# Kernel optimization log

Hardware: AMD Instinct MI355X
Metric: run time of the kernel (lower is better)

Reference implementation:

```python
import jax, jax.numpy as jnp
import numpy as np

EMBED = 256
HEADS = 8
LEVELS = 4
POINTS = 4
HD = EMBED // HEADS  # 32


def _bilinear_sample(v, grid):
    """torch.F.grid_sample(mode='bilinear', padding_mode='zeros', align_corners=False).
    v: (B, C, H, W); grid: (B, Q, P, 2) with xy coords in [-1, 1].
    Returns (B, C, Q, P).
    """
    B, C, H, W = v.shape
    x = (grid[..., 0] + 1.0) * (W * 0.5) - 0.5
    y = (grid[..., 1] + 1.0) * (H * 0.5) - 0.5
    x0f = jnp.floor(x)
    y0f = jnp.floor(y)
    wx = x - x0f
    wy = y - y0f
    x0 = x0f.astype(jnp.int32)
    y0 = y0f.astype(jnp.int32)
    vf = v.reshape(B, C, H * W)

    def corner(xi, yi, w):
        valid = (xi >= 0) & (xi < W) & (yi >= 0) & (yi < H)
        idx = jnp.clip(yi, 0, H - 1) * W + jnp.clip(xi, 0, W - 1)  # (B, Q, P)
        g = jax.vmap(lambda vb, ib: jnp.take(vb, ib, axis=1))(vf, idx.reshape(B, -1))
        g = g.reshape(B, C, idx.shape[1], idx.shape[2])  # (B, C, Q, P)
        return g * (w * valid.astype(v.dtype))[:, None]

    return (corner(x0, y0, (1 - wx) * (1 - wy))
            + corner(x0 + 1, y0, wx * (1 - wy))
            + corner(x0, y0 + 1, (1 - wx) * wy)
            + corner(x0 + 1, y0 + 1, wx * wy))


def setup_inputs() -> dict:
    key = jax.random.key(0)
    ks = jax.random.split(key, 16)
    N, Q, D = 2, 8192, EMBED
    inp = {
        'query': jax.random.normal(ks[0], (N, Q, D), jnp.float32),
        'feat0': jax.random.normal(ks[1], (N, D, 64, 64), jnp.float32),
        'feat1': jax.random.normal(ks[2], (N, D, 32, 32), jnp.float32),
        'feat2': jax.random.normal(ks[3], (N, D, 16, 16), jnp.float32),
        'feat3': jax.random.normal(ks[4], (N, D, 8, 8), jnp.float32),
        'reference_points': jax.random.uniform(ks[5], (N, Q, 2), jnp.float32),
        # params stored as (in, out); equivalent math to torch Linear's x @ W.T + b
        'W_off': jax.random.normal(ks[6], (D, HEADS * LEVELS * POINTS * 2), jnp.float32) * 0.01,
        'b_off': jax.random.normal(ks[7], (HEADS * LEVELS * POINTS * 2,), jnp.float32) * 0.01,
        'W_attn': jax.random.normal(ks[8], (D, HEADS * LEVELS * POINTS), jnp.float32) * 0.02,
        'b_attn': jax.random.normal(ks[9], (HEADS * LEVELS * POINTS,), jnp.float32) * 0.02,
        'W_val': jax.random.normal(ks[10], (D, D), jnp.float32) * (1.0 / np.sqrt(D)),
        'b_val': jnp.zeros((D,), jnp.float32),
        'W_out': jax.random.normal(ks[11], (D, D), jnp.float32) * (1.0 / np.sqrt(D)),
        'b_out': jnp.zeros((D,), jnp.float32),
    }
    return inp


def reference(query, feat0, feat1, feat2, feat3, reference_points,
              W_off, b_off, W_attn, b_attn, W_val, b_val, W_out, b_out):
    feats = [feat0, feat1, feat2, feat3]
    N, Q, D = query.shape
    # offset / attention-weight projections
    off = (query @ W_off + b_off).reshape(N, Q, HEADS, LEVELS, POINTS, 2)
    attn = (query @ W_attn + b_attn).reshape(N, Q, HEADS, LEVELS, POINTS)
    # reference points (N,Q,2) -> (N,Q,L,2)
    ref = jnp.broadcast_to(reference_points[:, :, None, :], (N, Q, LEVELS, 2))
    # value projection (1x1 conv) per level, split heads -> (N*H, hd, H_l, W_l)
    vals = [(jnp.einsum('bchw,cd->bdhw', f, W_val) + b_val[None, :, None, None])
            .reshape(N * HEADS, HD, f.shape[2], f.shape[3]) for f in feats]
    # flatten batch*heads
    off = off.transpose(0, 2, 1, 3, 4, 5).reshape(N * HEADS, Q, LEVELS, POINTS, 2)
    attn = attn.transpose(0, 2, 1, 3, 4).reshape(N * HEADS, Q, LEVELS, POINTS)
    refh = jnp.broadcast_to(ref[:, None], (N, HEADS, Q, LEVELS, 2)).reshape(N * HEADS, Q, LEVELS, 2)
    loc = refh[:, :, :, None, :] + off                 # (NH, Q, L, P, 2) in [0,1]
    grid = 2.0 * loc - 1.0                             # [-1, 1]
    # per-level bilinear sampling -> (NH, hd, Q, L, P)
    sampled = jnp.stack([_bilinear_sample(vals[l], grid[:, :, l]) for l in range(LEVELS)], axis=-2)
    # softmax over levels*points
    aw = jax.nn.softmax(attn.reshape(N * HEADS, Q, LEVELS * POINTS), axis=-1)
    aw = jnp.nan_to_num(aw).reshape(N * HEADS, Q, LEVELS, POINTS)
    out = jnp.einsum('bcqlp,bqlp->bcq', sampled, aw)   # (NH, hd, Q)
    out = out.reshape(N, HEADS, HD, Q).transpose(0, 3, 1, 2).reshape(N, Q, D)
    return out @ W_out + b_out
```

## Files before the change

### kernel.cpp

```cpp
#include <hip/hip_runtime.h>
#include <math.h>

#define NB 2
#define QN 8192
#define DIM 256
#define S_TOT 5440

typedef unsigned int uint32;
typedef _Float16 f16;
typedef __attribute__((ext_vector_type(8))) _Float16 h8;
typedef __attribute__((ext_vector_type(2))) _Float16 h2;
typedef __attribute__((ext_vector_type(4))) float f32x4;
typedef __attribute__((ext_vector_type(4))) uint32 u32x4;

__global__ __launch_bounds__(256) void prep_w_kernel(
    const float* __restrict__ W_off, const float* __restrict__ W_attn,
    const float* __restrict__ W_val, const float* __restrict__ W_out,
    f16* __restrict__ Wcat_t, f16* __restrict__ Wval_t, f16* __restrict__ Wout_t) {
  const int t = blockIdx.x;
  const float* src; f16* dst; int S, tb;
  if (t < 8)       { src = W_off;  dst = Wcat_t;           S = 256; tb = t; }
  else if (t < 12) { src = W_attn; dst = Wcat_t + 256*256; S = 128; tb = t - 8; }
  else if (t < 20) { src = W_val;  dst = Wval_t;           S = 256; tb = t - 12; }
  else             { src = W_out;  dst = Wout_t;           S = 256; tb = t - 20; }

  __shared__ float tile[32][33];
  const int tx = threadIdx.x & 31, ty = threadIdx.x >> 5;
  const int s0 = tb * 32, c0 = blockIdx.y * 32;
#pragma unroll
  for (int j = 0; j < 4; ++j) {
    const int c = c0 + ty + j * 8;
    tile[ty + j * 8][tx] = src[(size_t)c * S + s0 + tx];
  }
  __syncthreads();
#pragma unroll
  for (int j = 0; j < 4; ++j) {
    const int srow = s0 + ty + j * 8;
    dst[(size_t)srow * 256 + c0 + tx] = (f16)tile[tx][ty + j * 8];
  }
}

__global__ __launch_bounds__(256) void tconv_feat_kernel(
    const float* __restrict__ f0, const float* __restrict__ f1,
    const float* __restrict__ f2, const float* __restrict__ f3,
    f16* __restrict__ featT) {
  const int t = blockIdx.x, b = blockIdx.z, c0 = blockIdx.y * 32;
  const float* src; int HW, soff, tb;
  if (t < 128)      { src = f0; HW = 4096; soff = 0;    tb = t; }
  else if (t < 160) { src = f1; HW = 1024; soff = 4096; tb = t - 128; }
  else if (t < 168) { src = f2; HW = 256;  soff = 5120; tb = t - 160; }
  else              { src = f3; HW = 64;   soff = 5376; tb = t - 168; }
  const int s0 = tb * 32;

  __shared__ float tile[32][33];
  const int tx = threadIdx.x & 31, ty = threadIdx.x >> 5;
  const float* sp = src + (size_t)b * 256 * HW;
#pragma unroll
  for (int j = 0; j < 4; ++j) {
    const int c = c0 + ty + j * 8;
    tile[ty + j * 8][tx] = sp[(size_t)c * HW + s0 + tx];
  }
  __syncthreads();
#pragma unroll
  for (int j = 0; j < 4; ++j) {
    const int srow = s0 + ty + j * 8;
    featT[((size_t)b * S_TOT + soff + srow) * 256 + c0 + tx] =
        (f16)tile[tx][ty + j * 8];
  }
}

template <int MODE>
__global__ __launch_bounds__(256) void gemm_f16_kernel(
    const f16* __restrict__ A, const float* __restrict__ Af32,
    const f16* __restrict__ Bt,
    const float* __restrict__ bias0, const float* __restrict__ bias1,
    f16* __restrict__ o0, f16* __restrict__ o1, float* __restrict__ o2) {
  __shared__ f16 As[64][256];
  __shared__ f16 Bs[64][256];
  const int tid = threadIdx.x;
  const size_t r0 = (size_t)blockIdx.x * 64;
  const size_t c0 = (size_t)blockIdx.y * 64;

  {
    const f16* gb = Bt + c0 * 256;
    const int row = tid >> 5, slot = tid & 31;
#pragma unroll
    for (int i = 0; i < 8; ++i) {
      const int r = i * 8 + row;
      const int ph = (slot & 24) | ((slot ^ r) & 7);
      if constexpr (MODE == 1) {
        const float* ga = Af32 + (r0 + r) * 256 + slot * 8;
        const float4 u0 = *(const float4*)ga;
        const float4 u1 = *(const float4*)(ga + 4);
        h8 hv = {(f16)u0.x, (f16)u0.y, (f16)u0.z, (f16)u0.w,
                 (f16)u1.x, (f16)u1.y, (f16)u1.z, (f16)u1.w};
        *(h8*)&As[r][ph * 8] = hv;
      } else {
        *(u32x4*)&As[r][ph * 8] =
            *(const u32x4*)(A + (r0 + r) * 256 + slot * 8);
      }
      *(u32x4*)&Bs[r][ph * 8] = *(const u32x4*)(gb + (size_t)r * 256 + slot * 8);
    }
  }
  __syncthreads();

  const int wid = tid >> 6, lane = tid & 63;
  const int wr = (wid >> 1) * 32, wc = (wid & 1) * 32;
  const int l15 = lane & 15, l4 = lane >> 4;

  f32x4 acc[2][2] = {};
#pragma unroll
  for (int ks = 0; ks < 8; ++ks) {
    const int slot = ks * 4 + l4;
    h8 a[2], b[2];
#pragma unroll
    for (int m = 0; m < 2; ++m) {
      const int r = wr + m * 16 + l15;
      const int ph = (slot & 24) | ((slot ^ r) & 7);
      a[m] = *(const h8*)&As[r][ph * 8];
    }
#pragma unroll
    for (int n = 0; n < 2; ++n) {
      const int r = wc + n * 16 + l15;
      const int ph = (slot & 24) | ((slot ^ r) & 7);
      b[n] = *(const h8*)&Bs[r][ph * 8];
    }
#pragma unroll
    for (int m = 0; m < 2; ++m)
#pragma unroll
      for (int n = 0; n < 2; ++n)
        acc[m][n] = __builtin_amdgcn_mfma_f32_16x16x32_f16(a[m], b[n], acc[m][n], 0, 0, 0);
  }

#pragma unroll
  for (int m = 0; m < 2; ++m)
#pragma unroll
    for (int n = 0; n < 2; ++n)
#pragma unroll
      for (int r = 0; r < 4; ++r) {
        const size_t row = r0 + wr + m * 16 + l4 * 4 + r;
        const size_t col = c0 + wc + n * 16 + l15;
        const float v = acc[m][n][r];
        if constexpr (MODE == 0) {
          o0[row * 256 + col] = (f16)(v + bias0[col]);
        } else if constexpr (MODE == 1) {
          if (c0 < 256)
            o0[row * 256 + col] = (f16)(v + bias0[col]);
          else
            o1[row * 128 + (col - 256)] = (f16)(v + bias1[col - 256]);
        } else {
          o2[row * 256 + col] = v + bias0[col];
        }
      }
}

__global__ __launch_bounds__(256) void sample_kernel(
    const f16* __restrict__ vals, const f16* __restrict__ offb,
    const f16* __restrict__ attnb, const float* __restrict__ refp,
    f16* __restrict__ samp) {
  const int tid = threadIdx.x;
  const int g = tid & 15;
  const int grp = tid >> 4;
  const int h = grp & 7;
  const int half = tid >> 7;
  const int bq = blockIdx.x * 2 + half;
  const int b = bq >> 13;

  __shared__ float4 wts[16][17];
  __shared__ int4 idxs[16][17];

  const float rx = refp[(size_t)bq * 2 + 0];
  const float ry = refp[(size_t)bq * 2 + 1];

  float logit = (float)attnb[(size_t)bq * 128 + h * 16 + g];
  float m = logit;
#pragma unroll
  for (int mask = 1; mask < 16; mask <<= 1)
    m = fmaxf(m, __shfl_xor(m, mask, 16));
  const float e = __expf(logit - m);
  float ssum = e;
#pragma unroll
  for (int mask = 1; mask < 16; mask <<= 1)
    ssum += __shfl_xor(ssum, mask, 16);
  const float aw = e / ssum;

  const h2 ov = *(const h2*)(offb + (size_t)bq * 256 + h * 32 + g * 2);
  const int l = g >> 2;
  const int Wl = 64 >> l;
  const int loff = (l == 0) ? 0 : (l == 1) ? 4096 : (l == 2) ? 5120 : 5376;

  const float px = (rx + (float)ov[0]) * (float)Wl - 0.5f;
  const float py = (ry + (float)ov[1]) * (float)Wl - 0.5f;
  const float fx = floorf(px), fy = floorf(py);
  const float wx = px - fx, wy = py - fy;
  const int x0 = (int)fx, y0 = (int)fy;
  const int x1 = x0 + 1, y1 = y0 + 1;
  const float vx0 = (x0 >= 0 && x0 < Wl) ? 1.f : 0.f;
  const float vx1 = (x1 >= 0 && x1 < Wl) ? 1.f : 0.f;
  const float vy0 = (y0 >= 0 && y0 < Wl) ? 1.f : 0.f;
  const float vy1 = (y1 >= 0 && y1 < Wl) ? 1.f : 0.f;
  const int cx0 = min(max(x0, 0), Wl - 1), cx1 = min(max(x1, 0), Wl - 1);
  const int cy0 = min(max(y0, 0), Wl - 1), cy1 = min(max(y1, 0), Wl - 1);
  const int base = b * S_TOT + loff;
  idxs[grp][g] = make_int4((base + cy0 * Wl + cx0) * 512,
                           (base + cy0 * Wl + cx1) * 512,
                           (base + cy1 * Wl + cx0) * 512,
                           (base + cy1 * Wl + cx1) * 512);
  wts[grp][g] = make_float4(aw * (1.f - wx) * (1.f - wy) * vx0 * vy0,
                            aw * wx * (1.f - wy) * vx1 * vy0,
                            aw * (1.f - wx) * wy * vx0 * vy1,
                            aw * wx * wy * vx1 * vy1);
  __syncthreads();

  const int c4 = g & 3, pc = g >> 2;
  const char* vb = (const char*)vals + (h * 64 + c4 * 16);
  float a[8] = {};
#pragma unroll
  for (int pt = 0; pt < 16; ++pt) {
    const float w = ((const float*)&wts[grp][pt])[pc];
    const int id = ((const int*)&idxs[grp][pt])[pc];
    const h8 v = *(const h8*)(vb + id);
#pragma unroll
    for (int k = 0; k < 8; ++k) a[k] = fmaf((float)v[k], w, a[k]);
  }
#pragma unroll
  for (int k = 0; k < 8; ++k) {
    a[k] += __shfl_xor(a[k], 4);
    a[k] += __shfl_xor(a[k], 8);
  }
  if (pc == 0) {
    h8 r;
#pragma unroll
    for (int k = 0; k < 8; ++k) r[k] = (f16)a[k];
    *(h8*)(samp + (size_t)bq * 256 + h * 32 + c4 * 8) = r;
  }
}

extern "C" void kernel_launch(void* const* d_in, const int* in_sizes, int n_in,
                              void* d_out, int out_size, void* d_ws, size_t ws_size,
                              hipStream_t stream) {
  const float* query = (const float*)d_in[0];
  const float* feat[4] = {(const float*)d_in[1], (const float*)d_in[2],
                          (const float*)d_in[3], (const float*)d_in[4]};
  const float* refp  = (const float*)d_in[5];
  const float* W_off = (const float*)d_in[6];
  const float* b_off = (const float*)d_in[7];
  const float* W_attn = (const float*)d_in[8];
  const float* b_attn = (const float*)d_in[9];
  const float* W_val = (const float*)d_in[10];
  const float* b_val = (const float*)d_in[11];
  const float* W_out = (const float*)d_in[12];
  const float* b_out = (const float*)d_in[13];
  float* out = (float*)d_out;

  f16* ws = (f16*)d_ws;
  f16* featT  = ws;
  f16* attnb  = featT;
  f16* vals   = featT + (size_t)NB * S_TOT * 256;
  f16* offb   = vals + (size_t)NB * S_TOT * 256;
  f16* samp   = offb + (size_t)NB * QN * 256;
  f16* Wcat_t = samp + (size_t)NB * QN * 256;
  f16* Wval_t = Wcat_t + 384 * 256;
  f16* Wout_t = Wval_t + 256 * 256;

  prep_w_kernel<<<dim3(28, 8, 1), 256, 0, stream>>>(
      W_off, W_attn, W_val, W_out, Wcat_t, Wval_t, Wout_t);
  tconv_feat_kernel<<<dim3(170, 8, NB), 256, 0, stream>>>(
      feat[0], feat[1], feat[2], feat[3], featT);

  gemm_f16_kernel<0><<<dim3((NB * S_TOT) / 64, 4), 256, 0, stream>>>(
      featT, nullptr, Wval_t, b_val, nullptr, vals, nullptr, nullptr);

  gemm_f16_kernel<1><<<dim3((NB * QN) / 64, 6), 256, 0, stream>>>(
      nullptr, query, Wcat_t, b_off, b_attn, offb, attnb, nullptr);

  sample_kernel<<<(NB * QN) / 2, 256, 0, stream>>>(vals, offb, attnb, refp, samp);

  gemm_f16_kernel<2><<<dim3((NB * QN) / 64, 4), 256, 0, stream>>>(
      samp, nullptr, Wout_t, b_out, nullptr, nullptr, nullptr, out);
}
```

Before: 77.60 us.

## Merge prep and projection GEMM launches, batch sampler gathers before accumulation

Folds the weight-transpose and feature-transpose kernels into one launch, and the value-projection and offset/attention GEMMs into one launch using a flat block index. This removes two kernel launches and the idle gaps between them, letting the two independent GEMMs share the GPU. The sampler now loads all 16 gathered vectors into registers before accumulating, exposing more memory-level parallelism at the cost of registers. attnb also gets its own workspace region instead of aliasing featT, which is required now that both GEMMs run concurrently.

```diff
diff --git a/kernel.cpp b/kernel.cpp
--- a/kernel.cpp
+++ b/kernel.cpp
@@ -13,20 +13,38 @@
 typedef __attribute__((ext_vector_type(4))) float f32x4;
 typedef __attribute__((ext_vector_type(4))) uint32 u32x4;
 
-__global__ __launch_bounds__(256) void prep_w_kernel(
+__global__ __launch_bounds__(256) void prep_kernel(
+    const float* __restrict__ f0, const float* __restrict__ f1,
+    const float* __restrict__ f2, const float* __restrict__ f3,
     const float* __restrict__ W_off, const float* __restrict__ W_attn,
     const float* __restrict__ W_val, const float* __restrict__ W_out,
-    f16* __restrict__ Wcat_t, f16* __restrict__ Wval_t, f16* __restrict__ Wout_t) {
+    f16* __restrict__ featT, f16* __restrict__ Wcat_t,
+    f16* __restrict__ Wval_t, f16* __restrict__ Wout_t) {
   const int t = blockIdx.x;
-  const float* src; f16* dst; int S, tb;
-  if (t < 8)       { src = W_off;  dst = Wcat_t;           S = 256; tb = t; }
-  else if (t < 12) { src = W_attn; dst = Wcat_t + 256*256; S = 128; tb = t - 8; }
-  else if (t < 20) { src = W_val;  dst = Wval_t;           S = 256; tb = t - 12; }
-  else             { src = W_out;  dst = Wout_t;           S = 256; tb = t - 20; }
+  const float* src;
+  f16* dst;
+  int S, tb;
+  if (t < 340) {
+    const int b = (t >= 170) ? 1 : 0;
+    const int tt = t - 170 * b;
+    int soff;
+    if (tt < 128)      { src = f0; S = 4096; soff = 0;    tb = tt; }
+    else if (tt < 160) { src = f1; S = 1024; soff = 4096; tb = tt - 128; }
+    else if (tt < 168) { src = f2; S = 256;  soff = 5120; tb = tt - 160; }
+    else               { src = f3; S = 64;   soff = 5376; tb = tt - 168; }
+    src += (size_t)b * 256 * S;
+    dst = featT + ((size_t)b * S_TOT + soff) * 256;
+  } else {
+    const int tw = t - 340;
+    if (tw < 8)       { src = W_off;  dst = Wcat_t;             S = 256; tb = tw; }
+    else if (tw < 12) { src = W_attn; dst = Wcat_t + 256 * 256; S = 128; tb = tw - 8; }
+    else if (tw < 20) { src = W_val;  dst = Wval_t;             S = 256; tb = tw - 12; }
+    else              { src = W_out;  dst = Wout_t;             S = 256; tb = tw - 20; }
+  }
+  const int s0 = tb * 32, c0 = blockIdx.y * 32;
 
   __shared__ float tile[32][33];
   const int tx = threadIdx.x & 31, ty = threadIdx.x >> 5;
-  const int s0 = tb * 32, c0 = blockIdx.y * 32;
 #pragma unroll
   for (int j = 0; j < 4; ++j) {
     const int c = c0 + ty + j * 8;
@@ -40,41 +58,96 @@
   }
 }
 
-__global__ __launch_bounds__(256) void tconv_feat_kernel(
-    const float* __restrict__ f0, const float* __restrict__ f1,
-    const float* __restrict__ f2, const float* __restrict__ f3,
-    f16* __restrict__ featT) {
-  const int t = blockIdx.x, b = blockIdx.z, c0 = blockIdx.y * 32;
-  const float* src; int HW, soff, tb;
-  if (t < 128)      { src = f0; HW = 4096; soff = 0;    tb = t; }
-  else if (t < 160) { src = f1; HW = 1024; soff = 4096; tb = t - 128; }
-  else if (t < 168) { src = f2; HW = 256;  soff = 5120; tb = t - 160; }
-  else              { src = f3; HW = 64;   soff = 5376; tb = t - 168; }
-  const int s0 = tb * 32;
-
-  __shared__ float tile[32][33];
-  const int tx = threadIdx.x & 31, ty = threadIdx.x >> 5;
-  const float* sp = src + (size_t)b * 256 * HW;
-#pragma unroll
-  for (int j = 0; j < 4; ++j) {
-    const int c = c0 + ty + j * 8;
-    tile[ty + j * 8][tx] = sp[(size_t)c * HW + s0 + tx];
+__global__ __launch_bounds__(256) void gemm_fused_kernel(
+    const f16* __restrict__ featT, const float* __restrict__ query,
+    const f16* __restrict__ Wval_t, const f16* __restrict__ Wcat_t,
+    const float* __restrict__ b_val, const float* __restrict__ b_off,
+    const float* __restrict__ b_attn,
+    f16* __restrict__ vals, f16* __restrict__ offb, f16* __restrict__ attnb) {
+  __shared__ f16 As[64][256];
+  __shared__ f16 Bs[64][256];
+  const int t = blockIdx.x;
+  const int tid = threadIdx.x;
+  const bool isval = (t < 680);
+  size_t r0, c0;
+  const f16* Bt;
+  if (isval) { r0 = (size_t)(t >> 2) * 64;      c0 = (size_t)(t & 3) * 64;  Bt = Wval_t; }
+  else       { const int t2 = t - 680;
+               r0 = (size_t)(t2 / 6) * 64;      c0 = (size_t)(t2 % 6) * 64; Bt = Wcat_t; }
+
+  {
+    const f16* gb = Bt + c0 * 256;
+    const int row = tid >> 5, slot = tid & 31;
+#pragma unroll
+    for (int i = 0; i < 8; ++i) {
+      const int r = i * 8 + row;
+      const int ph = (slot & 24) | ((slot ^ r) & 7);
+      if (isval) {
+        *(u32x4*)&As[r][ph * 8] =
+            *(const u32x4*)(featT + (r0 + r) * 256 + slot * 8);
+      } else {
+        const float* ga = query + (r0 + r) * 256 + slot * 8;
+        const float4 u0 = *(const float4*)ga;
+        const float4 u1 = *(const float4*)(ga + 4);
+        h8 hv = {(f16)u0.x, (f16)u0.y, (f16)u0.z, (f16)u0.w,
+                 (f16)u1.x, (f16)u1.y, (f16)u1.z, (f16)u1.w};
+        *(h8*)&As[r][ph * 8] = hv;
+      }
+      *(u32x4*)&Bs[r][ph * 8] = *(const u32x4*)(gb + (size_t)r * 256 + slot * 8);
+    }
   }
   __syncthreads();
-#pragma unroll
-  for (int j = 0; j < 4; ++j) {
-    const int srow = s0 + ty + j * 8;
-    featT[((size_t)b * S_TOT + soff + srow) * 256 + c0 + tx] =
-        (f16)tile[tx][ty + j * 8];
-  }
-}
-
-template <int MODE>
-__global__ __launch_bounds__(256) void gemm_f16_kernel(
-    const f16* __restrict__ A, const float* __restrict__ Af32,
-    const f16* __restrict__ Bt,
-    const float* __restrict__ bias0, const float* __restrict__ bias1,
-    f16* __restrict__ o0, f16* __restrict__ o1, float* __restrict__ o2) {
+
+  const int wid = tid >> 6, lane = tid & 63;
+  const int wr = (wid >> 1) * 32, wc = (wid & 1) * 32;
+  const int l15 = lane & 15, l4 = lane >> 4;
+
+  f32x4 acc[2][2] = {};
+#pragma unroll
+  for (int ks = 0; ks < 8; ++ks) {
+    const int slot = ks * 4 + l4;
+    h8 a[2], b[2];
+#pragma unroll
+    for (int m = 0; m < 2; ++m) {
+      const int r = wr + m * 16 + l15;
+      const int ph = (slot & 24) | ((slot ^ r) & 7);
+      a[m] = *(const h8*)&As[r][ph * 8];
+    }
+#pragma unroll
+    for (int n = 0; n < 2; ++n) {
+      const int r = wc + n * 16 + l15;
+      const int ph = (slot & 24) | ((slot ^ r) & 7);
+      b[n] = *(const h8*)&Bs[r][ph * 8];
+    }
+#pragma unroll
+    for (int m = 0; m < 2; ++m)
+#pragma unroll
+      for (int n = 0; n < 2; ++n)
+        acc[m][n] = __builtin_amdgcn_mfma_f32_16x16x32_f16(a[m], b[n], acc[m][n], 0, 0, 0);
+  }
+
+#pragma unroll
+  for (int m = 0; m < 2; ++m)
+#pragma unroll
+    for (int n = 0; n < 2; ++n)
+#pragma unroll
+      for (int r = 0; r < 4; ++r) {
+        const size_t row = r0 + wr + m * 16 + l4 * 4 + r;
+        const size_t col = c0 + wc + n * 16 + l15;
+        const float v = acc[m][n][r];
+        if (isval) {
+          vals[row * 256 + col] = (f16)(v + b_val[col]);
+        } else if (c0 < 256) {
+          offb[row * 256 + col] = (f16)(v + b_off[col]);
+        } else {
+          attnb[row * 128 + (col - 256)] = (f16)(v + b_attn[col - 256]);
+        }
+      }
+}
+
+__global__ __launch_bounds__(256) void gemm_out_kernel(
+    const f16* __restrict__ A, const f16* __restrict__ Bt,
+    const float* __restrict__ bias, float* __restrict__ out) {
   __shared__ f16 As[64][256];
   __shared__ f16 Bs[64][256];
   const int tid = threadIdx.x;
@@ -82,23 +155,14 @@
   const size_t c0 = (size_t)blockIdx.y * 64;
 
   {
+    const f16* ga = A + r0 * 256;
     const f16* gb = Bt + c0 * 256;
     const int row = tid >> 5, slot = tid & 31;
 #pragma unroll
     for (int i = 0; i < 8; ++i) {
       const int r = i * 8 + row;
       const int ph = (slot & 24) | ((slot ^ r) & 7);
-      if constexpr (MODE == 1) {
-        const float* ga = Af32 + (r0 + r) * 256 + slot * 8;
-        const float4 u0 = *(const float4*)ga;
-        const float4 u1 = *(const float4*)(ga + 4);
-        h8 hv = {(f16)u0.x, (f16)u0.y, (f16)u0.z, (f16)u0.w,
-                 (f16)u1.x, (f16)u1.y, (f16)u1.z, (f16)u1.w};
-        *(h8*)&As[r][ph * 8] = hv;
-      } else {
-        *(u32x4*)&As[r][ph * 8] =
-            *(const u32x4*)(A + (r0 + r) * 256 + slot * 8);
-      }
+      *(u32x4*)&As[r][ph * 8] = *(const u32x4*)(ga + (size_t)r * 256 + slot * 8);
       *(u32x4*)&Bs[r][ph * 8] = *(const u32x4*)(gb + (size_t)r * 256 + slot * 8);
     }
   }
@@ -140,17 +204,7 @@
       for (int r = 0; r < 4; ++r) {
         const size_t row = r0 + wr + m * 16 + l4 * 4 + r;
         const size_t col = c0 + wc + n * 16 + l15;
-        const float v = acc[m][n][r];
-        if constexpr (MODE == 0) {
-          o0[row * 256 + col] = (f16)(v + bias0[col]);
-        } else if constexpr (MODE == 1) {
-          if (c0 < 256)
-            o0[row * 256 + col] = (f16)(v + bias0[col]);
-          else
-            o1[row * 128 + (col - 256)] = (f16)(v + bias1[col - 256]);
-        } else {
-          o2[row * 256 + col] = v + bias0[col];
-        }
+        out[row * 256 + col] = acc[m][n][r] + bias[col];
       }
 }
 
@@ -214,14 +268,23 @@
 
   const int c4 = g & 3, pc = g >> 2;
   const char* vb = (const char*)vals + (h * 64 + c4 * 16);
+
+  float wv[16];
+  int ids[16];
+#pragma unroll
+  for (int pt = 0; pt < 16; ++pt) {
+    wv[pt] = ((const float*)&wts[grp][pt])[pc];
+    ids[pt] = ((const int*)&idxs[grp][pt])[pc];
+  }
+  h8 vv[16];
+#pragma unroll
+  for (int pt = 0; pt < 16; ++pt) vv[pt] = *(const h8*)(vb + ids[pt]);
+
   float a[8] = {};
 #pragma unroll
   for (int pt = 0; pt < 16; ++pt) {
-    const float w = ((const float*)&wts[grp][pt])[pc];
-    const int id = ((const int*)&idxs[grp][pt])[pc];
-    const h8 v = *(const h8*)(vb + id);
-#pragma unroll
-    for (int k = 0; k < 8; ++k) a[k] = fmaf((float)v[k], w, a[k]);
+#pragma unroll
+    for (int k = 0; k < 8; ++k) a[k] = fmaf((float)vv[pt][k], wv[pt], a[k]);
   }
 #pragma unroll
   for (int k = 0; k < 8; ++k) {
@@ -255,27 +318,23 @@
 
   f16* ws = (f16*)d_ws;
   f16* featT  = ws;
-  f16* attnb  = featT;
   f16* vals   = featT + (size_t)NB * S_TOT * 256;
   f16* offb   = vals + (size_t)NB * S_TOT * 256;
   f16* samp   = offb + (size_t)NB * QN * 256;
-  f16* Wcat_t = samp + (size_t)NB * QN * 256;
+  f16* attnb  = samp + (size_t)NB * QN * 256;
+  f16* Wcat_t = attnb + (size_t)NB * QN * 128;
   f16* Wval_t = Wcat_t + 384 * 256;
   f16* Wout_t = Wval_t + 256 * 256;
 
-  prep_w_kernel<<<dim3(28, 8, 1), 256, 0, stream>>>(
-      W_off, W_attn, W_val, W_out, Wcat_t, Wval_t, Wout_t);
-  tconv_feat_kernel<<<dim3(170, 8, NB), 256, 0, stream>>>(
-      feat[0], feat[1], feat[2], feat[3], featT);
-
-  gemm_f16_kernel<0><<<dim3((NB * S_TOT) / 64, 4), 256, 0, stream>>>(
-      featT, nullptr, Wval_t, b_val, nullptr, vals, nullptr, nullptr);
-
-  gemm_f16_kernel<1><<<dim3((NB * QN) / 64, 6), 256, 0, stream>>>(
-      nullptr, query, Wcat_t, b_off, b_attn, offb, attnb, nullptr);
+  prep_kernel<<<dim3(368, 8), 256, 0, stream>>>(
+      feat[0], feat[1], feat[2], feat[3], W_off, W_attn, W_val, W_out,
+      featT, Wcat_t, Wval_t, Wout_t);
+
+  gemm_fused_kernel<<<680 + 1536, 256, 0, stream>>>(
+      featT, query, Wval_t, Wcat_t, b_val, b_off, b_attn, vals, offb, attnb);
 
   sample_kernel<<<(NB * QN) / 2, 256, 0, stream>>>(vals, offb, attnb, refp, samp);
 
-  gemm_f16_kernel<2><<<dim3((NB * QN) / 64, 4), 256, 0, stream>>>(
-      samp, nullptr, Wout_t, b_out, nullptr, nullptr, nullptr, out);
-}
+  gemm_out_kernel<<<dim3((NB * QN) / 64, 4), 256, 0, stream>>>(
+      samp, Wout_t, b_out, out);
+}
```

Result: slower. 80.98 us (+4.4%).
